# Kernel tuning notes

Hardware: AMD Instinct MI355X
Metric: run time of the kernel (lower is better)

Reference implementation:

```python
import jax, jax.numpy as jnp
import numpy as np

B, S, DIM, NH = 4, 2048, 2048, 16
HD = DIM // NH  # 128


def setup_inputs() -> dict:
    key = jax.random.key(0)
    ks = jax.random.split(key, 6)
    x = jax.random.normal(ks[0], (B, S, DIM), dtype=jnp.float32)
    wq = jax.random.normal(ks[1], (DIM, DIM), dtype=jnp.float32) * (DIM ** -0.5)
    wk = jax.random.normal(ks[2], (DIM, DIM), dtype=jnp.float32) * (DIM ** -0.5)
    wv = jax.random.normal(ks[3], (DIM, DIM), dtype=jnp.float32) * (DIM ** -0.5)
    wo = jax.random.normal(ks[4], (DIM, DIM), dtype=jnp.float32) * (DIM ** -0.5)
    # RoPE frequencies: theta^{-2i/hd}, angle = pos * freq
    inv_freq = 1.0 / (10000.0 ** (np.arange(0, HD, 2, dtype=np.float32) / HD))  # [HD/2]
    angles = np.arange(S, dtype=np.float32)[:, None] * inv_freq[None, :]  # [S, HD/2]
    freqs_cos = jnp.asarray(np.cos(angles))
    freqs_sin = jnp.asarray(np.sin(angles))
    # causal mask, additive [S, S]
    mask = jnp.where(jnp.tril(jnp.ones((S, S), dtype=bool)), 0.0, -jnp.inf).astype(jnp.float32)
    return {"x": x, "wq": wq, "wk": wk, "wv": wv, "wo": wo,
            "freqs_cos": freqs_cos, "freqs_sin": freqs_sin, "mask": mask,
            "start_pos": 0}


def _apply_rotary(xq, xk, cos, sin):
    # xq, xk: [B, S, H, HD]; cos/sin: [S, HD/2]
    def rot(t):
        tr = t.reshape(*t.shape[:-1], -1, 2)  # [B,S,H,HD/2,2]
        a, b = tr[..., 0], tr[..., 1]
        c = cos[None, :, None, :]
        s = sin[None, :, None, :]
        # complex multiply (a+ib)(c+is)
        out = jnp.stack([a * c - b * s, a * s + b * c], axis=-1)
        return out.reshape(t.shape)
    return rot(xq), rot(xk)


def reference(x, wq, wk, wv, wo, freqs_cos, freqs_sin, mask, start_pos):
    bsz, seqlen, _ = x.shape
    # nn.Linear: y = x @ W^T
    xq = (x @ wq.T).reshape(bsz, seqlen, NH, HD)
    xk = (x @ wk.T).reshape(bsz, seqlen, NH, HD)
    xv = (x @ wv.T).reshape(bsz, seqlen, NH, HD)
    xq, xk = _apply_rotary(xq, xk, freqs_cos, freqs_sin)
    # attention, heads to axis 1
    scores = jnp.einsum('bqhd,bkhd->bhqk', xq, xk) / jnp.sqrt(jnp.float32(HD))
    scores = scores + mask[None, None, :, :]
    probs = jax.nn.softmax(scores.astype(jnp.float32), axis=-1).astype(xq.dtype)
    out = jnp.einsum('bhqk,bkhd->bqhd', probs, xv).reshape(bsz, seqlen, -1)
    return out @ wo.T
```

## Files before the change

kernel.cpp:

```cpp
#include <hip/hip_runtime.h>

typedef __attribute__((ext_vector_type(8))) __bf16 bf16x8;
typedef __attribute__((ext_vector_type(4))) float f32x4;
typedef __attribute__((ext_vector_type(16))) float f32x16;
typedef __attribute__((ext_vector_type(8))) unsigned short u16x8;
typedef __attribute__((ext_vector_type(2))) unsigned uint2v;

#define LOG2E 1.44269504088896340736f

__device__ __forceinline__ unsigned short f2bf(float f){
  union { float f; unsigned u; } v; v.f = f;
  unsigned r = v.u + 0x7FFFu + ((v.u >> 16) & 1u);
  return (unsigned short)(r >> 16);
}
__device__ __forceinline__ float bf2f(unsigned short u){
  union { unsigned u; float f; } v; v.u = ((unsigned)u) << 16;
  return v.f;
}

typedef const unsigned __attribute__((address_space(1)))* gas_ptr;
typedef unsigned __attribute__((address_space(3)))* las_ptr;

__device__ __forceinline__ void gload_lds16(const void* g, void* l){
  __builtin_amdgcn_global_load_lds((gas_ptr)g, (las_ptr)l, 16, 0, 0);
}

__device__ __forceinline__ unsigned cvtpk(float lo, float hi){
  unsigned r;
  asm("v_cvt_pk_bf16_f32 %0, %1, %2" : "=v"(r) : "v"(lo), "v"(hi));
  return r;
}
__device__ __forceinline__ void swap32(unsigned &a, unsigned &b){
  uint2v r = __builtin_amdgcn_permlane32_swap(a, b, false, false);
  a = r[0]; b = r[1];
}

__global__ __launch_bounds__(256) void cvt_f32_bf16(const float* __restrict__ in,
                                                    unsigned short* __restrict__ out){
  size_t i = ((size_t)blockIdx.x * 256 + threadIdx.x) * 4;
  float4 vv = *(const float4*)(in + i);
  ushort4 o;
  o.x = f2bf(vv.x); o.y = f2bf(vv.y); o.z = f2bf(vv.z); o.w = f2bf(vv.w);
  *(ushort4*)(out + i) = o;
}

#define BUF(op, half, par) (LDS + (((op) * 2 + (half)) * 2 + (par)) * 16384)

#define STAGE(op, gbase, half, par, kt) do {                                   \
  _Pragma("unroll")                                                            \
  for (int c_ = 0; c_ < 2; ++c_){                                              \
    int slot_ = c_ * 512 + w * 64 + l;                                         \
    int row_ = slot_ >> 3, colb_ = slot_ & 7;                                  \
    gload_lds16((const char*)((gbase) + (size_t)((half) * 128 + row_) * K +    \
                              (size_t)(kt) * 64 + ((colb_ ^ (row_ & 7)) * 8)), \
                BUF(op, half, par) + c_ * 8192 + w * 1024);                    \
  } } while (0)

#define PHASE(mh, nh, par, ...) do {                                           \
  bf16x8 af_[4][2], bf_[2][2];                                                 \
  const char* Ab_ = BUF(0, mh, par);                                           \
  const char* Bb_ = BUF(1, nh, par);                                           \
  _Pragma("unroll")                                                            \
  for (int i_ = 0; i_ < 4; ++i_){                                              \
    int row_ = wm * 64 + i_ * 16 + lq;                                         \
    _Pragma("unroll")                                                          \
    for (int ks_ = 0; ks_ < 2; ++ks_)                                          \
      af_[i_][ks_] = *(const bf16x8*)(Ab_ + row_ * 128 +                       \
                                      (((ks_ * 4 + lg) ^ (row_ & 7)) * 16));   \
  }                                                                            \
  _Pragma("unroll")                                                            \
  for (int j_ = 0; j_ < 2; ++j_){                                              \
    int row_ = wn * 32 + j_ * 16 + lq;                                         \
    _Pragma("unroll")                                                          \
    for (int ks_ = 0; ks_ < 2; ++ks_)                                          \
      bf_[j_][ks_] = *(const bf16x8*)(Bb_ + row_ * 128 +                       \
                                      (((ks_ * 4 + lg) ^ (row_ & 7)) * 16));   \
  }                                                                            \
  __VA_ARGS__;                                                                 \
  __builtin_amdgcn_s_barrier();                                                \
  asm volatile("s_waitcnt lgkmcnt(0)");                                        \
  __builtin_amdgcn_s_setprio(1);                                               \
  _Pragma("unroll")                                                            \
  for (int i_ = 0; i_ < 4; ++i_)                                               \
    _Pragma("unroll")                                                          \
    for (int j_ = 0; j_ < 2; ++j_)                                             \
      _Pragma("unroll")                                                        \
      for (int ks_ = 0; ks_ < 2; ++ks_)                                        \
        acc[(mh) * 4 + i_][(nh) * 2 + j_] = __builtin_amdgcn_mfma_f32_16x16x32_bf16( \
            af_[i_][ks_], bf_[j_][ks_], acc[(mh) * 4 + i_][(nh) * 2 + j_], 0, 0, 0); \
  __builtin_amdgcn_s_setprio(0);                                               \
  __builtin_amdgcn_s_barrier();                                                \
} while (0)

template<bool OUT_BF16, bool ROPE>
__global__ __launch_bounds__(512, 2) void gemm256(const unsigned short* __restrict__ A,
                                                  const unsigned short* __restrict__ B,
                                                  void* __restrict__ Cv,
                                                  int M, int N, int K,
                                                  const float* __restrict__ fc,
                                                  const float* __restrict__ fs){
  __shared__ char LDS[131072];
  const int tid = threadIdx.x;
  const int l = tid & 63, w = tid >> 6;
  const int lq = l & 15, lg = l >> 4;
  const int wm = w >> 2, wn = w & 3;

  const int nwg = gridDim.x, cpx = nwg >> 3;
  const int orig = blockIdx.x;
  const int sw = (orig & 7) * cpx + (orig >> 3);
  const int nbc = N >> 8;
  const int br = sw / nbc, bc = sw % nbc;

  f32x4 acc[8][4] = {};
  const unsigned short* Ag = A + (size_t)br * 256 * K;
  const unsigned short* Bg = B + (size_t)bc * 256 * K;
  const int NT = K >> 6;

  STAGE(0, Ag, 0, 0, 0); STAGE(1, Bg, 0, 0, 0);
  STAGE(0, Ag, 1, 0, 0); STAGE(1, Bg, 1, 0, 0);
  STAGE(1, Bg, 0, 1, 1); STAGE(0, Ag, 0, 1, 1);
  asm volatile("s_waitcnt vmcnt(4)" ::: "memory");
  __builtin_amdgcn_s_barrier();

  for (int t = 0; t < NT; ++t){
    const int par = t & 1, parn = par ^ 1;
    PHASE(0, 0, par, { if (t + 1 < NT) STAGE(0, Ag, 1, parn, t + 1); });
    PHASE(1, 0, par, { if (t + 1 < NT) STAGE(1, Bg, 1, parn, t + 1); });
    PHASE(0, 1, par, { if (t + 2 < NT) STAGE(1, Bg, 0, par, t + 2); });
    PHASE(1, 1, par, { if (t + 2 < NT) STAGE(0, Ag, 0, par, t + 2); });
    asm volatile("s_waitcnt vmcnt(4)" ::: "memory");
    __builtin_amdgcn_s_barrier();
  }

#pragma unroll
  for (int i = 0; i < 8; ++i){
    int grow = br * 256 + (i >> 2) * 128 + wm * 64 + (i & 3) * 16 + lg * 4;
#pragma unroll
    for (int j = 0; j < 4; ++j){
      int gcol = bc * 256 + (j >> 1) * 128 + wn * 32 + (j & 1) * 16 + lq;
#pragma unroll
      for (int r = 0; r < 4; ++r){
        float v = acc[i][j][r];
        if (ROPE){
          int s = (grow + r) & 2047;
          int i0 = (gcol & 127) >> 1;
          float cc = fc[s * 64 + i0], sn = fs[s * 64 + i0];
          float part = __shfl_xor(v, 1, 64);
          v = (lq & 1) ? __builtin_fmaf(part, sn, v * cc)
                       : __builtin_fmaf(-part, sn, v * cc);
        }
        if (OUT_BF16)
          ((unsigned short*)Cv)[(size_t)(grow + r) * N + gcol] = f2bf(v);
        else
          ((float*)Cv)[(size_t)(grow + r) * N + gcol] = v;
      }
    }
  }
}

__global__ __launch_bounds__(512, 2) void attn_fwd(const unsigned short* __restrict__ Q,
                                                   const unsigned short* __restrict__ K,
                                                   const unsigned short* __restrict__ V,
                                                   unsigned short* __restrict__ O){
  __shared__ unsigned short SMEM[2 * 64 * 128 + 2 * 128 * 64];
  unsigned short* Ks = SMEM;
  unsigned short* Vt = SMEM + 16384;

  const int tid = threadIdx.x;
  const int l = tid & 63, wid = tid >> 6;
  const int lq = l & 31, hi = l >> 5;
  const int bh = blockIdx.x & 63;
  const int pair = blockIdx.x >> 6;
  const int b = bh >> 4, h = bh & 15;
  const float c2 = 0.12751743f;

  const int dblk = tid >> 5, kvp = tid & 31;
  const size_t hb = (size_t)b * 2048 * 2048 + (size_t)h * 128;

  for (int strip = 0; strip < 2; ++strip){
    const int qt = strip == 0 ? pair : 7 - pair;
    const int qw = qt * 256 + wid * 32;

    const unsigned short* qptr = Q + ((size_t)(b * 2048 + qw + lq)) * 2048 + (size_t)h * 128;
    bf16x8 qf[8];
#pragma unroll
    for (int ks = 0; ks < 8; ++ks)
      qf[ks] = *(const bf16x8*)(qptr + ks * 16 + hi * 8);

    f32x16 oacc[4];
#pragma unroll
    for (int i = 0; i < 4; ++i)
#pragma unroll
      for (int j = 0; j < 16; ++j) oacc[i][j] = 0.f;
    float mrow = -3.0e38f, lrow = 0.f;
    u16x8 r0, r1;

    {
      const size_t kvb = hb;
#pragma unroll
      for (int c = 0; c < 2; ++c){
        int off = c * 8192 + tid * 16;
        int row = off >> 8, colb = off & 255;
        gload_lds16((const char*)(K + kvb + (size_t)row * 2048) + (colb ^ ((row & 15) << 4)),
                    (char*)Ks + c * 8192 + (tid >> 6) * 1024 + (tid & 63) * 16);
      }
      const unsigned short* vp = V + kvb + (size_t)(2 * kvp) * 2048 + dblk * 8;
      r0 = *(const u16x8*)vp; r1 = *(const u16x8*)(vp + 2048);
      asm volatile("s_waitcnt vmcnt(0)" ::: "memory");
#pragma unroll
      for (int j = 0; j < 8; ++j){
        int d = dblk * 8 + j;
        unsigned val = (unsigned)r0[j] | ((unsigned)r1[j] << 16);
        *(unsigned*)((char*)Vt + d * 128 + ((4 * kvp) ^ ((d & 7) << 4))) = val;
      }
    }
    __syncthreads();

    const int nkt = 4 * qt + 4;
    for (int kt = 0; kt < nkt; ++kt){
      const int cur = kt & 1, nxt = cur ^ 1;
      const bool pref = (kt + 1 < nkt);
      char* KsC = (char*)(Ks + cur * 8192);
      char* VtC = (char*)(Vt + cur * 8192);

      if (pref){
        const size_t kvb = hb + (size_t)((kt + 1) * 64) * 2048;
        char* KsN = (char*)(Ks + nxt * 8192);
#pragma unroll
        for (int c = 0; c < 2; ++c){
          int off = c * 8192 + tid * 16;
          int row = off >> 8, colb = off & 255;
          gload_lds16((const char*)(K + kvb + (size_t)row * 2048) + (colb ^ ((row & 15) << 4)),
                      KsN + c * 8192 + (tid >> 6) * 1024 + (tid & 63) * 16);
        }
        const unsigned short* vp = V + kvb + (size_t)(2 * kvp) * 2048 + dblk * 8;
        r0 = *(const u16x8*)vp; r1 = *(const u16x8*)(vp + 2048);
      }

      if (!(kt * 64 > qw + 31)){
        f32x16 sacc[2];
#pragma unroll
        for (int sub = 0; sub < 2; ++sub){
#pragma unroll
          for (int j = 0; j < 16; ++j) sacc[sub][j] = 0.f;
          const int row = sub * 32 + lq;
          const int swz = (row & 15) << 4;
#pragma unroll
          for (int ks = 0; ks < 8; ++ks){
            bf16x8 kf = *(const bf16x8*)(KsC + row * 256 + ((ks * 32 + hi * 16) ^ swz));
            sacc[sub] = __builtin_amdgcn_mfma_f32_32x32x16_bf16(kf, qf[ks], sacc[sub], 0, 0, 0);
          }
        }

        float s[32];
#pragma unroll
        for (int sub = 0; sub < 2; ++sub)
#pragma unroll
          for (int r = 0; r < 16; ++r) s[sub * 16 + r] = sacc[sub][r];

        if (kt * 64 + 63 > qw){
          const int qg = qw + lq;
#pragma unroll
          for (int sub = 0; sub < 2; ++sub)
#pragma unroll
            for (int r = 0; r < 16; ++r){
              int kvg = kt * 64 + sub * 32 + (r & 3) + 8 * (r >> 2) + 4 * hi;
              if (kvg > qg) s[sub * 16 + r] = -3.0e38f;
            }
        }

        float mx[32];
#pragma unroll
        for (int i = 0; i < 32; ++i) mx[i] = s[i];
#pragma unroll
        for (int st = 1; st < 32; st <<= 1)
#pragma unroll
          for (int i = 0; i < 32; i += 2 * st) mx[i] = fmaxf(mx[i], mx[i + st]);
        float pmax = mx[0];
        pmax = fmaxf(pmax, __shfl_xor(pmax, 32, 64));

        float mm;
        if (__all((pmax - mrow) * c2 <= 8.0f)){
          mm = mrow * c2;
        } else {
          float mnew = fmaxf(mrow, pmax);
          mm = mnew * c2;
          float corr = __builtin_amdgcn_exp2f(__builtin_fmaf(mrow, c2, -mm));
          mrow = mnew;
          lrow *= corr;
#pragma unroll
          for (int i = 0; i < 4; ++i)
#pragma unroll
            for (int j = 0; j < 16; ++j) oacc[i][j] *= corr;
        }

        float p[32];
#pragma unroll
        for (int i = 0; i < 32; ++i)
          p[i] = __builtin_amdgcn_exp2f(__builtin_fmaf(s[i], c2, -mm));
        float sm[32];
#pragma unroll
        for (int i = 0; i < 32; ++i) sm[i] = p[i];
#pragma unroll
        for (int st = 1; st < 32; st <<= 1)
#pragma unroll
          for (int i = 0; i < 32; i += 2 * st) sm[i] += sm[i + st];
        float rs = sm[0];
        rs += __shfl_xor(rs, 32, 64);
        lrow += rs;

        unsigned wv[16];
#pragma unroll
        for (int i = 0; i < 16; ++i) wv[i] = cvtpk(p[2 * i], p[2 * i + 1]);
        swap32(wv[0], wv[2]);   swap32(wv[1], wv[3]);
        swap32(wv[4], wv[6]);   swap32(wv[5], wv[7]);
        swap32(wv[8], wv[10]);  swap32(wv[9], wv[11]);
        swap32(wv[12], wv[14]); swap32(wv[13], wv[15]);

#pragma unroll
        for (int c = 0; c < 4; ++c){
          union { unsigned u[4]; bf16x8 v; } pu;
          pu.u[0] = wv[c * 4 + 0]; pu.u[1] = wv[c * 4 + 1];
          pu.u[2] = wv[c * 4 + 2]; pu.u[3] = wv[c * 4 + 3];
#pragma unroll
          for (int db = 0; db < 4; ++db){
            const int d = db * 32 + lq;
            bf16x8 vf = *(const bf16x8*)(VtC + d * 128 + ((c * 32 + hi * 16) ^ ((d & 7) << 4)));
            oacc[db] = __builtin_amdgcn_mfma_f32_32x32x16_bf16(vf, pu.v, oacc[db], 0, 0, 0);
          }
        }
      }

      if (pref){
        asm volatile("s_waitcnt vmcnt(0)" ::: "memory");
        char* VtN = (char*)(Vt + nxt * 8192);
#pragma unroll
        for (int j = 0; j < 8; ++j){
          int d = dblk * 8 + j;
          unsigned val = (unsigned)r0[j] | ((unsigned)r1[j] << 16);
          *(unsigned*)(VtN + d * 128 + ((4 * kvp) ^ ((d & 7) << 4))) = val;
        }
      }
      __syncthreads();
    }

    float inv = 1.0f / lrow;
    char* lb = (char*)SMEM + wid * 8192;
#pragma unroll
    for (int db = 0; db < 4; ++db)
#pragma unroll
      for (int r = 0; r < 16; r += 2){
        int d = db * 32 + (r & 3) + 8 * (r >> 2) + 4 * hi;
        unsigned val = (unsigned)f2bf(oacc[db][r] * inv) |
                       ((unsigned)f2bf(oacc[db][r + 1] * inv) << 16);
        *(unsigned*)(lb + lq * 256 + ((2 * d) ^ ((lq & 7) << 4))) = val;
      }
    __syncthreads();
#pragma unroll
    for (int i = 0; i < 8; ++i){
      int rowq = i * 4 + (l >> 4);
      u16x8 vv = *(const u16x8*)(lb + rowq * 256 + (((l & 15) * 16) ^ ((rowq & 7) << 4)));
      *(u16x8*)(O + ((size_t)(b * 2048 + qw + rowq)) * 2048 + (size_t)h * 128 + (l & 15) * 8) = vv;
    }
    __syncthreads();
  }
}

extern "C" void kernel_launch(void* const* d_in, const int* in_sizes, int n_in,
                              void* d_out, int out_size, void* d_ws, size_t ws_size,
                              hipStream_t stream){
  const float* x  = (const float*)d_in[0];
  const float* wq = (const float*)d_in[1];
  const float* wk = (const float*)d_in[2];
  const float* wv = (const float*)d_in[3];
  const float* wo = (const float*)d_in[4];
  const float* fc = (const float*)d_in[5];
  const float* fs = (const float*)d_in[6];
  float* out = (float*)d_out;
  (void)in_sizes; (void)n_in; (void)out_size; (void)ws_size;

  const size_t XN = (size_t)8192 * 2048;
  const size_t WN = (size_t)2048 * 2048;

  unsigned short* xb  = (unsigned short*)d_ws;
  unsigned short* wqb = xb + XN;
  unsigned short* wkb = wqb + WN;
  unsigned short* wvb = wkb + WN;
  unsigned short* wob = wvb + WN;
  unsigned short* q   = wob + WN;
  unsigned short* k   = q + XN;
  unsigned short* v   = k + XN;
  unsigned short* att = xb;

  cvt_f32_bf16<<<dim3((unsigned)(XN / 1024)), 256, 0, stream>>>(x, xb);
  cvt_f32_bf16<<<dim3((unsigned)(WN / 1024)), 256, 0, stream>>>(wq, wqb);
  cvt_f32_bf16<<<dim3((unsigned)(WN / 1024)), 256, 0, stream>>>(wk, wkb);
  cvt_f32_bf16<<<dim3((unsigned)(WN / 1024)), 256, 0, stream>>>(wv, wvb);
  cvt_f32_bf16<<<dim3((unsigned)(WN / 1024)), 256, 0, stream>>>(wo, wob);

  gemm256<true, true ><<<dim3(256), 512, 0, stream>>>(xb, wqb, q, 8192, 2048, 2048, fc, fs);
  gemm256<true, true ><<<dim3(256), 512, 0, stream>>>(xb, wkb, k, 8192, 2048, 2048, fc, fs);
  gemm256<true, false><<<dim3(256), 512, 0, stream>>>(xb, wvb, v, 8192, 2048, 2048, nullptr, nullptr);

  attn_fwd<<<dim3(256), 512, 0, stream>>>(q, k, v, att);

  gemm256<false, false><<<dim3(256), 512, 0, stream>>>(att, wob, out, 8192, 2048, 2048, nullptr, nullptr);
}
```

Baseline: 463.5 us.

## Split attention strip pairs into separate blocks and reuse operand fragments in GEMM

The attention kernel previously paired two query strips (qt and 7-qt) per block to balance causal work. Now each block handles one strip, ordered longest-first, and the grid doubles to 512 blocks. The aim is more parallelism and better tail behaviour, at the cost of relying on the hardware scheduler for load balance. Separately, the GEMM main loop now reads the A and B LDS fragments once and reuses them across MFMA phases, cutting redundant LDS reads at the cost of more live registers.

```diff
diff --git a/kernel.cpp b/kernel.cpp
--- a/kernel.cpp
+++ b/kernel.cpp
@@ -56,27 +56,29 @@
                 BUF(op, half, par) + c_ * 8192 + w * 1024);                    \
   } } while (0)
 
-#define PHASE(mh, nh, par, ...) do {                                           \
-  bf16x8 af_[4][2], bf_[2][2];                                                 \
-  const char* Ab_ = BUF(0, mh, par);                                           \
-  const char* Bb_ = BUF(1, nh, par);                                           \
+#define RD_A(buf) do {                                                         \
+  const char* Ab_ = (buf);                                                     \
   _Pragma("unroll")                                                            \
   for (int i_ = 0; i_ < 4; ++i_){                                              \
     int row_ = wm * 64 + i_ * 16 + lq;                                         \
     _Pragma("unroll")                                                          \
     for (int ks_ = 0; ks_ < 2; ++ks_)                                          \
-      af_[i_][ks_] = *(const bf16x8*)(Ab_ + row_ * 128 +                       \
-                                      (((ks_ * 4 + lg) ^ (row_ & 7)) * 16));   \
-  }                                                                            \
+      aA[i_][ks_] = *(const bf16x8*)(Ab_ + row_ * 128 +                        \
+                                     (((ks_ * 4 + lg) ^ (row_ & 7)) * 16));    \
+  } } while (0)
+
+#define RD_B(buf, arr) do {                                                    \
+  const char* Bb_ = (buf);                                                     \
   _Pragma("unroll")                                                            \
   for (int j_ = 0; j_ < 2; ++j_){                                              \
     int row_ = wn * 32 + j_ * 16 + lq;                                         \
     _Pragma("unroll")                                                          \
     for (int ks_ = 0; ks_ < 2; ++ks_)                                          \
-      bf_[j_][ks_] = *(const bf16x8*)(Bb_ + row_ * 128 +                       \
+      arr[j_][ks_] = *(const bf16x8*)(Bb_ + row_ * 128 +                       \
                                       (((ks_ * 4 + lg) ^ (row_ & 7)) * 16));   \
-  }                                                                            \
-  __VA_ARGS__;                                                                 \
+  } } while (0)
+
+#define DO_MFMA(mh, nh, arr) do {                                              \
   __builtin_amdgcn_s_barrier();                                                \
   asm volatile("s_waitcnt lgkmcnt(0)");                                        \
   __builtin_amdgcn_s_setprio(1);                                               \
@@ -87,7 +89,7 @@
       _Pragma("unroll")                                                        \
       for (int ks_ = 0; ks_ < 2; ++ks_)                                        \
         acc[(mh) * 4 + i_][(nh) * 2 + j_] = __builtin_amdgcn_mfma_f32_16x16x32_bf16( \
-            af_[i_][ks_], bf_[j_][ks_], acc[(mh) * 4 + i_][(nh) * 2 + j_], 0, 0, 0); \
+            aA[i_][ks_], arr[j_][ks_], acc[(mh) * 4 + i_][(nh) * 2 + j_], 0, 0, 0); \
   __builtin_amdgcn_s_setprio(0);                                               \
   __builtin_amdgcn_s_barrier();                                                \
 } while (0)
@@ -112,6 +114,7 @@
   const int br = sw / nbc, bc = sw % nbc;
 
   f32x4 acc[8][4] = {};
+  bf16x8 aA[4][2], bB0[2][2], bB1[2][2];
   const unsigned short* Ag = A + (size_t)br * 256 * K;
   const unsigned short* Bg = B + (size_t)bc * 256 * K;
   const int NT = K >> 6;
@@ -124,10 +127,18 @@
 
   for (int t = 0; t < NT; ++t){
     const int par = t & 1, parn = par ^ 1;
-    PHASE(0, 0, par, { if (t + 1 < NT) STAGE(0, Ag, 1, parn, t + 1); });
-    PHASE(1, 0, par, { if (t + 1 < NT) STAGE(1, Bg, 1, parn, t + 1); });
-    PHASE(0, 1, par, { if (t + 2 < NT) STAGE(1, Bg, 0, par, t + 2); });
-    PHASE(1, 1, par, { if (t + 2 < NT) STAGE(0, Ag, 0, par, t + 2); });
+    RD_A(BUF(0, 0, par));
+    RD_B(BUF(1, 0, par), bB0);
+    if (t + 1 < NT) STAGE(0, Ag, 1, parn, t + 1);
+    DO_MFMA(0, 0, bB0);
+    RD_B(BUF(1, 1, par), bB1);
+    if (t + 1 < NT) STAGE(1, Bg, 1, parn, t + 1);
+    DO_MFMA(0, 1, bB1);
+    RD_A(BUF(0, 1, par));
+    if (t + 2 < NT) STAGE(0, Ag, 0, par, t + 2);
+    DO_MFMA(1, 0, bB0);
+    if (t + 2 < NT) STAGE(1, Bg, 0, par, t + 2);
+    DO_MFMA(1, 1, bB1);
     asm volatile("s_waitcnt vmcnt(4)" ::: "memory");
     __builtin_amdgcn_s_barrier();
   }
@@ -170,199 +181,194 @@
   const int l = tid & 63, wid = tid >> 6;
   const int lq = l & 31, hi = l >> 5;
   const int bh = blockIdx.x & 63;
-  const int pair = blockIdx.x >> 6;
+  const int qt = 7 - (blockIdx.x >> 6);
   const int b = bh >> 4, h = bh & 15;
+  const int qw = qt * 256 + wid * 32;
   const float c2 = 0.12751743f;
+
+  const unsigned short* qptr = Q + ((size_t)(b * 2048 + qw + lq)) * 2048 + (size_t)h * 128;
+  bf16x8 qf[8];
+#pragma unroll
+  for (int ks = 0; ks < 8; ++ks)
+    qf[ks] = *(const bf16x8*)(qptr + ks * 16 + hi * 8);
+
+  f32x16 oacc[4];
+#pragma unroll
+  for (int i = 0; i < 4; ++i)
+#pragma unroll
+    for (int j = 0; j < 16; ++j) oacc[i][j] = 0.f;
+  float mrow = -3.0e38f, lrow = 0.f;
 
   const int dblk = tid >> 5, kvp = tid & 31;
   const size_t hb = (size_t)b * 2048 * 2048 + (size_t)h * 128;
-
-  for (int strip = 0; strip < 2; ++strip){
-    const int qt = strip == 0 ? pair : 7 - pair;
-    const int qw = qt * 256 + wid * 32;
-
-    const unsigned short* qptr = Q + ((size_t)(b * 2048 + qw + lq)) * 2048 + (size_t)h * 128;
-    bf16x8 qf[8];
-#pragma unroll
-    for (int ks = 0; ks < 8; ++ks)
-      qf[ks] = *(const bf16x8*)(qptr + ks * 16 + hi * 8);
-
-    f32x16 oacc[4];
-#pragma unroll
-    for (int i = 0; i < 4; ++i)
-#pragma unroll
-      for (int j = 0; j < 16; ++j) oacc[i][j] = 0.f;
-    float mrow = -3.0e38f, lrow = 0.f;
-    u16x8 r0, r1;
-
-    {
-      const size_t kvb = hb;
+  u16x8 r0, r1;
+
+  {
+    const size_t kvb = hb;
+#pragma unroll
+    for (int c = 0; c < 2; ++c){
+      int off = c * 8192 + tid * 16;
+      int row = off >> 8, colb = off & 255;
+      gload_lds16((const char*)(K + kvb + (size_t)row * 2048) + (colb ^ ((row & 15) << 4)),
+                  (char*)Ks + c * 8192 + (tid >> 6) * 1024 + (tid & 63) * 16);
+    }
+    const unsigned short* vp = V + kvb + (size_t)(2 * kvp) * 2048 + dblk * 8;
+    r0 = *(const u16x8*)vp; r1 = *(const u16x8*)(vp + 2048);
+    asm volatile("s_waitcnt vmcnt(0)" ::: "memory");
+#pragma unroll
+    for (int j = 0; j < 8; ++j){
+      int d = dblk * 8 + j;
+      unsigned val = (unsigned)r0[j] | ((unsigned)r1[j] << 16);
+      *(unsigned*)((char*)Vt + d * 128 + ((4 * kvp) ^ ((d & 7) << 4))) = val;
+    }
+  }
+  __syncthreads();
+
+  const int nkt = 4 * qt + 4;
+  for (int kt = 0; kt < nkt; ++kt){
+    const int cur = kt & 1, nxt = cur ^ 1;
+    const bool pref = (kt + 1 < nkt);
+    char* KsC = (char*)(Ks + cur * 8192);
+    char* VtC = (char*)(Vt + cur * 8192);
+
+    if (pref){
+      const size_t kvb = hb + (size_t)((kt + 1) * 64) * 2048;
+      char* KsN = (char*)(Ks + nxt * 8192);
 #pragma unroll
       for (int c = 0; c < 2; ++c){
         int off = c * 8192 + tid * 16;
         int row = off >> 8, colb = off & 255;
         gload_lds16((const char*)(K + kvb + (size_t)row * 2048) + (colb ^ ((row & 15) << 4)),
-                    (char*)Ks + c * 8192 + (tid >> 6) * 1024 + (tid & 63) * 16);
+                    KsN + c * 8192 + (tid >> 6) * 1024 + (tid & 63) * 16);
       }
       const unsigned short* vp = V + kvb + (size_t)(2 * kvp) * 2048 + dblk * 8;
       r0 = *(const u16x8*)vp; r1 = *(const u16x8*)(vp + 2048);
+    }
+
+    if (!(kt * 64 > qw + 31)){
+      f32x16 sacc[2];
+#pragma unroll
+      for (int sub = 0; sub < 2; ++sub){
+#pragma unroll
+        for (int j = 0; j < 16; ++j) sacc[sub][j] = 0.f;
+        const int row = sub * 32 + lq;
+        const int swz = (row & 15) << 4;
+#pragma unroll
+        for (int ks = 0; ks < 8; ++ks){
+          bf16x8 kf = *(const bf16x8*)(KsC + row * 256 + ((ks * 32 + hi * 16) ^ swz));
+          sacc[sub] = __builtin_amdgcn_mfma_f32_32x32x16_bf16(kf, qf[ks], sacc[sub], 0, 0, 0);
+        }
+      }
+
+      float s[32];
+#pragma unroll
+      for (int sub = 0; sub < 2; ++sub)
+#pragma unroll
+        for (int r = 0; r < 16; ++r) s[sub * 16 + r] = sacc[sub][r];
+
+      if (kt * 64 + 63 > qw){
+        const int qg = qw + lq;
+#pragma unroll
+        for (int sub = 0; sub < 2; ++sub)
+#pragma unroll
+          for (int r = 0; r < 16; ++r){
+            int kvg = kt * 64 + sub * 32 + (r & 3) + 8 * (r >> 2) + 4 * hi;
+            if (kvg > qg) s[sub * 16 + r] = -3.0e38f;
+          }
+      }
+
+      float mx[32];
+#pragma unroll
+      for (int i = 0; i < 32; ++i) mx[i] = s[i];
+#pragma unroll
+      for (int st = 1; st < 32; st <<= 1)
+#pragma unroll
+        for (int i = 0; i < 32; i += 2 * st) mx[i] = fmaxf(mx[i], mx[i + st]);
+      float pmax = mx[0];
+      pmax = fmaxf(pmax, __shfl_xor(pmax, 32, 64));
+
+      float mm;
+      if (__all((pmax - mrow) * c2 <= 8.0f)){
+        mm = mrow * c2;
+      } else {
+        float mnew = fmaxf(mrow, pmax);
+        mm = mnew * c2;
+        float corr = __builtin_amdgcn_exp2f(__builtin_fmaf(mrow, c2, -mm));
+        mrow = mnew;
+        lrow *= corr;
+#pragma unroll
+        for (int i = 0; i < 4; ++i)
+#pragma unroll
+          for (int j = 0; j < 16; ++j) oacc[i][j] *= corr;
+      }
+
+      float p[32];
+#pragma unroll
+      for (int i = 0; i < 32; ++i)
+        p[i] = __builtin_amdgcn_exp2f(__builtin_fmaf(s[i], c2, -mm));
+      float sm[32];
+#pragma unroll
+      for (int i = 0; i < 32; ++i) sm[i] = p[i];
+#pragma unroll
+      for (int st = 1; st < 32; st <<= 1)
+#pragma unroll
+        for (int i = 0; i < 32; i += 2 * st) sm[i] += sm[i + st];
+      float rs = sm[0];
+      rs += __shfl_xor(rs, 32, 64);
+      lrow += rs;
+
+      unsigned wv[16];
+#pragma unroll
+      for (int i = 0; i < 16; ++i) wv[i] = cvtpk(p[2 * i], p[2 * i + 1]);
+      swap32(wv[0], wv[2]);   swap32(wv[1], wv[3]);
+      swap32(wv[4], wv[6]);   swap32(wv[5], wv[7]);
+      swap32(wv[8], wv[10]);  swap32(wv[9], wv[11]);
+      swap32(wv[12], wv[14]); swap32(wv[13], wv[15]);
+
+#pragma unroll
+      for (int c = 0; c < 4; ++c){
+        union { unsigned u[4]; bf16x8 v; } pu;
+        pu.u[0] = wv[c * 4 + 0]; pu.u[1] = wv[c * 4 + 1];
+        pu.u[2] = wv[c * 4 + 2]; pu.u[3] = wv[c * 4 + 3];
+#pragma unroll
+        for (int db = 0; db < 4; ++db){
+          const int d = db * 32 + lq;
+          bf16x8 vf = *(const bf16x8*)(VtC + d * 128 + ((c * 32 + hi * 16) ^ ((d & 7) << 4)));
+          oacc[db] = __builtin_amdgcn_mfma_f32_32x32x16_bf16(vf, pu.v, oacc[db], 0, 0, 0);
+        }
+      }
+    }
+
+    if (pref){
       asm volatile("s_waitcnt vmcnt(0)" ::: "memory");
+      char* VtN = (char*)(Vt + nxt * 8192);
 #pragma unroll
       for (int j = 0; j < 8; ++j){
         int d = dblk * 8 + j;
         unsigned val = (unsigned)r0[j] | ((unsigned)r1[j] << 16);
-        *(unsigned*)((char*)Vt + d * 128 + ((4 * kvp) ^ ((d & 7) << 4))) = val;
+        *(unsigned*)(VtN + d * 128 + ((4 * kvp) ^ ((d & 7) << 4))) = val;
       }
     }
     __syncthreads();
-
-    const int nkt = 4 * qt + 4;
-    for (int kt = 0; kt < nkt; ++kt){
-      const int cur = kt & 1, nxt = cur ^ 1;
-      const bool pref = (kt + 1 < nkt);
-      char* KsC = (char*)(Ks + cur * 8192);
-      char* VtC = (char*)(Vt + cur * 8192);
-
-      if (pref){
-        const size_t kvb = hb + (size_t)((kt + 1) * 64) * 2048;
-        char* KsN = (char*)(Ks + nxt * 8192);
-#pragma unroll
-        for (int c = 0; c < 2; ++c){
-          int off = c * 8192 + tid * 16;
-          int row = off >> 8, colb = off & 255;
-          gload_lds16((const char*)(K + kvb + (size_t)row * 2048) + (colb ^ ((row & 15) << 4)),
-                      KsN + c * 8192 + (tid >> 6) * 1024 + (tid & 63) * 16);
-        }
-        const unsigned short* vp = V + kvb + (size_t)(2 * kvp) * 2048 + dblk * 8;
-        r0 = *(const u16x8*)vp; r1 = *(const u16x8*)(vp + 2048);
-      }
-
-      if (!(kt * 64 > qw + 31)){
-        f32x16 sacc[2];
-#pragma unroll
-        for (int sub = 0; sub < 2; ++sub){
-#pragma unroll
-          for (int j = 0; j < 16; ++j) sacc[sub][j] = 0.f;
-          const int row = sub * 32 + lq;
-          const int swz = (row & 15) << 4;
-#pragma unroll
-          for (int ks = 0; ks < 8; ++ks){
-            bf16x8 kf = *(const bf16x8*)(KsC + row * 256 + ((ks * 32 + hi * 16) ^ swz));
-            sacc[sub] = __builtin_amdgcn_mfma_f32_32x32x16_bf16(kf, qf[ks], sacc[sub], 0, 0, 0);
-          }
-        }
-
-        float s[32];
-#pragma unroll
-        for (int sub = 0; sub < 2; ++sub)
-#pragma unroll
-          for (int r = 0; r < 16; ++r) s[sub * 16 + r] = sacc[sub][r];
-
-        if (kt * 64 + 63 > qw){
-          const int qg = qw + lq;
-#pragma unroll
-          for (int sub = 0; sub < 2; ++sub)
-#pragma unroll
-            for (int r = 0; r < 16; ++r){
-              int kvg = kt * 64 + sub * 32 + (r & 3) + 8 * (r >> 2) + 4 * hi;
-              if (kvg > qg) s[sub * 16 + r] = -3.0e38f;
-            }
-        }
-
-        float mx[32];
-#pragma unroll
-        for (int i = 0; i < 32; ++i) mx[i] = s[i];
-#pragma unroll
-        for (int st = 1; st < 32; st <<= 1)
-#pragma unroll
-          for (int i = 0; i < 32; i += 2 * st) mx[i] = fmaxf(mx[i], mx[i + st]);
-        float pmax = mx[0];
-        pmax = fmaxf(pmax, __shfl_xor(pmax, 32, 64));
-
-        float mm;
-        if (__all((pmax - mrow) * c2 <= 8.0f)){
-          mm = mrow * c2;
-        } else {
-          float mnew = fmaxf(mrow, pmax);
-          mm = mnew * c2;
-          float corr = __builtin_amdgcn_exp2f(__builtin_fmaf(mrow, c2, -mm));
-          mrow = mnew;
-          lrow *= corr;
-#pragma unroll
-          for (int i = 0; i < 4; ++i)
-#pragma unroll
-            for (int j = 0; j < 16; ++j) oacc[i][j] *= corr;
-        }
-
-        float p[32];
-#pragma unroll
-        for (int i = 0; i < 32; ++i)
-          p[i] = __builtin_amdgcn_exp2f(__builtin_fmaf(s[i], c2, -mm));
-        float sm[32];
-#pragma unroll
-        for (int i = 0; i < 32; ++i) sm[i] = p[i];
-#pragma unroll
-        for (int st = 1; st < 32; st <<= 1)
-#pragma unroll
-          for (int i = 0; i < 32; i += 2 * st) sm[i] += sm[i + st];
-        float rs = sm[0];
-        rs += __shfl_xor(rs, 32, 64);
-        lrow += rs;
-
-        unsigned wv[16];
-#pragma unroll
-        for (int i = 0; i < 16; ++i) wv[i] = cvtpk(p[2 * i], p[2 * i + 1]);
-        swap32(wv[0], wv[2]);   swap32(wv[1], wv[3]);
-        swap32(wv[4], wv[6]);   swap32(wv[5], wv[7]);
-        swap32(wv[8], wv[10]);  swap32(wv[9], wv[11]);
-        swap32(wv[12], wv[14]); swap32(wv[13], wv[15]);
-
-#pragma unroll
-        for (int c = 0; c < 4; ++c){
-          union { unsigned u[4]; bf16x8 v; } pu;
-          pu.u[0] = wv[c * 4 + 0]; pu.u[1] = wv[c * 4 + 1];
-          pu.u[2] = wv[c * 4 + 2]; pu.u[3] = wv[c * 4 + 3];
-#pragma unroll
-          for (int db = 0; db < 4; ++db){
-            const int d = db * 32 + lq;
-            bf16x8 vf = *(const bf16x8*)(VtC + d * 128 + ((c * 32 + hi * 16) ^ ((d & 7) << 4)));
-            oacc[db] = __builtin_amdgcn_mfma_f32_32x32x16_bf16(vf, pu.v, oacc[db], 0, 0, 0);
-          }
-        }
-      }
-
-      if (pref){
-        asm volatile("s_waitcnt vmcnt(0)" ::: "memory");
-        char* VtN = (char*)(Vt + nxt * 8192);
-#pragma unroll
-        for (int j = 0; j < 8; ++j){
-          int d = dblk * 8 + j;
-          unsigned val = (unsigned)r0[j] | ((unsigned)r1[j] << 16);
-          *(unsigned*)(VtN + d * 128 + ((4 * kvp) ^ ((d & 7) << 4))) = val;
-        }
-      }
-      __syncthreads();
-    }
-
-    float inv = 1.0f / lrow;
-    char* lb = (char*)SMEM + wid * 8192;
-#pragma unroll
-    for (int db = 0; db < 4; ++db)
-#pragma unroll
-      for (int r = 0; r < 16; r += 2){
-        int d = db * 32 + (r & 3) + 8 * (r >> 2) + 4 * hi;
-        unsigned val = (unsigned)f2bf(oacc[db][r] * inv) |
-                       ((unsigned)f2bf(oacc[db][r + 1] * inv) << 16);
-        *(unsigned*)(lb + lq * 256 + ((2 * d) ^ ((lq & 7) << 4))) = val;
-      }
-    __syncthreads();
-#pragma unroll
-    for (int i = 0; i < 8; ++i){
-      int rowq = i * 4 + (l >> 4);
-      u16x8 vv = *(const u16x8*)(lb + rowq * 256 + (((l & 15) * 16) ^ ((rowq & 7) << 4)));
-      *(u16x8*)(O + ((size_t)(b * 2048 + qw + rowq)) * 2048 + (size_t)h * 128 + (l & 15) * 8) = vv;
-    }
-    __syncthreads();
+  }
+
+  float inv = 1.0f / lrow;
+  char* lb = (char*)SMEM + wid * 8192;
+#pragma unroll
+  for (int db = 0; db < 4; ++db)
+#pragma unroll
+    for (int r = 0; r < 16; r += 2){
+      int d = db * 32 + (r & 3) + 8 * (r >> 2) + 4 * hi;
+      unsigned val = (unsigned)f2bf(oacc[db][r] * inv) |
+                     ((unsigned)f2bf(oacc[db][r + 1] * inv) << 16);
+      *(unsigned*)(lb + lq * 256 + ((2 * d) ^ ((lq & 7) << 4))) = val;
+    }
+  __syncthreads();
+#pragma unroll
+  for (int i = 0; i < 8; ++i){
+    int rowq = i * 4 + (l >> 4);
+    u16x8 vv = *(const u16x8*)(lb + rowq * 256 + (((l & 15) * 16) ^ ((rowq & 7) << 4)));
+    *(u16x8*)(O + ((size_t)(b * 2048 + qw + rowq)) * 2048 + (size_t)h * 128 + (l & 15) * 8) = vv;
   }
 }
 
@@ -402,7 +408,7 @@
   gemm256<true, true ><<<dim3(256), 512, 0, stream>>>(xb, wkb, k, 8192, 2048, 2048, fc, fs);
   gemm256<true, false><<<dim3(256), 512, 0, stream>>>(xb, wvb, v, 8192, 2048, 2048, nullptr, nullptr);
 
-  attn_fwd<<<dim3(256), 512, 0, stream>>>(q, k, v, att);
+  attn_fwd<<<dim3(512), 512, 0, stream>>>(q, k, v, att);
 
   gemm256<false, false><<<dim3(256), 512, 0, stream>>>(att, wob, out, 8192, 2048, 2048, nullptr, nullptr);
 }
```

Measured after the change: 407.3 us. 1.14x faster.
